# Optimization experiments

Hardware: AMD Instinct MI355X
Metric: run time of the kernel (lower is better)

## Reference

```python
import jax, jax.numpy as jnp
import numpy as np
import math

B, L, D, E, H = 8, 128, 512, 64, 8
SLOPE = 0.2
EPS = 1e-5


def setup_inputs() -> dict:
    key = jax.random.key(0)
    ks = jax.random.split(key, 10)
    s = 0.02
    x = jax.random.normal(ks[0], (B, L, D), jnp.float32)
    adj = jax.random.randint(ks[1], (B, L, L), 0, 2, jnp.int32)  # 0/1 adjacency
    e = jax.random.normal(ks[2], (B, L, L, E), jnp.float32)
    Wq = jax.random.normal(ks[3], (D, D), jnp.float32) * s
    Wkv = jax.random.normal(ks[4], (D, D), jnp.float32) * s
    We = jax.random.normal(ks[5], (E, D), jnp.float32) * s
    Wf = jax.random.normal(ks[6], (D, D), jnp.float32) * s
    bf = jnp.zeros((D,), jnp.float32)
    gamma = jnp.ones((D,), jnp.float32)
    beta = jnp.zeros((D,), jnp.float32)
    return {"x": x, "adj": adj, "e": e, "Wq": Wq, "Wkv": Wkv, "We": We,
            "Wf": Wf, "bf": bf, "gamma": gamma, "beta": beta}


def reference(x, adj, e, Wq, Wkv, We, Wf, bf, gamma, beta):
    C = D // H
    # projections
    q = (x @ Wq).reshape(B, L, H, C).transpose(0, 2, 1, 3)    # (B,H,L,C)
    kv = (x @ Wkv).reshape(B, L, H, C).transpose(0, 2, 1, 3)  # (B,H,L,C)
    ee = (e @ We).reshape(B, L, L, H, C).transpose(0, 3, 1, 2, 4)  # (B,H,Lq,Lk,C)
    # edge-modulated value/key: depends on both query and key position
    kve = kv[:, :, None, :, :] + ee                            # (B,H,Lq,Lk,C)
    # scores
    alpha = jnp.einsum('bhqc,bhqkc->bhqk', q, kve) / math.sqrt(C)
    alpha = jax.nn.leaky_relu(alpha, SLOPE)
    mask = (adj != 0)[:, None, :, :]                           # (B,1,Lq,Lk)
    alpha = jnp.where(mask, alpha, jnp.float32(-1e9))
    alpha = jax.nn.softmax(alpha, axis=-1)                     # over keys
    # weighted sum of edge-modulated values
    out = jnp.einsum('bhqk,bhqkc->bhqc', alpha, kve)           # (B,H,L,C)
    out = out.transpose(0, 2, 1, 3).reshape(B, L, D)
    # FFN: Linear -> LayerNorm -> ReLU
    out = out @ Wf + bf
    mu = out.mean(-1, keepdims=True)
    var = ((out - mu) ** 2).mean(-1, keepdims=True)
    out = (out - mu) / jnp.sqrt(var + EPS) * gamma + beta
    return jax.nn.relu(out)
```

## Files before the change

kernel.cpp:

```cpp
#include <hip/hip_runtime.h>
#include <hip/hip_bf16.h>
#include <math.h>

#define BB 8
#define LL 128
#define DD 512
#define EE 64
#define HH 8
#define CC 64
#define SLOPE 0.2f
#define EPS 1e-5f

typedef short bf16x8v __attribute__((ext_vector_type(8)));
typedef float f32x4v __attribute__((ext_vector_type(4)));

static __device__ __forceinline__ unsigned short f2bf(float f) {
    union { float f; unsigned u; } v; v.f = f;
    unsigned r = v.u + 0x7FFFu + ((v.u >> 16) & 1u);
    return (unsigned short)(r >> 16);
}

__global__ __launch_bounds__(256) void pack_all(
    const float* __restrict__ x, const float* __restrict__ Wq,
    const float* __restrict__ Wkv, const float* __restrict__ Wf,
    const float* __restrict__ We,
    unsigned short* __restrict__ xb, unsigned short* __restrict__ Wqkv_t,
    unsigned short* __restrict__ Wf_t, unsigned short* __restrict__ We_bf,
    unsigned short* __restrict__ WeT_bf)
{
    const int blk = blockIdx.x, tid = threadIdx.x;
    if (blk < 256) {
        const int j = blk * 512 + tid * 2;
        #pragma unroll
        for (int i = 0; i < 2; ++i) {
            const float4 v = ((const float4*)x)[j + i];
            ushort4 u; u.x = f2bf(v.x); u.y = f2bf(v.y); u.z = f2bf(v.z); u.w = f2bf(v.w);
            ((ushort4*)xb)[j + i] = u;
        }
    } else if (blk < 1024) {
        __shared__ float tile[32][33];
        const int matId = (blk - 256) >> 8;
        const int t = (blk - 256) & 255;
        const float* src = matId == 0 ? Wq : (matId == 1 ? Wkv : Wf);
        unsigned short* dst = matId == 0 ? Wqkv_t : (matId == 1 ? Wqkv_t + DD * DD : Wf_t);
        const int xx = tid & 31, yy = tid >> 5;
        const int r0 = (t >> 4) * 32, c0 = (t & 15) * 32;
        #pragma unroll
        for (int j = 0; j < 32; j += 8)
            tile[yy + j][xx] = src[(r0 + yy + j) * DD + c0 + xx];
        __syncthreads();
        #pragma unroll
        for (int j = 0; j < 32; j += 8)
            dst[(c0 + yy + j) * DD + r0 + xx] = f2bf(tile[xx][yy + j]);
    } else if (blk < 1040) {
        const int j = (blk - 1024) * 512 + tid * 2;
        #pragma unroll
        for (int i = 0; i < 2; ++i) {
            const float4 v = ((const float4*)We)[j + i];
            ushort4 u; u.x = f2bf(v.x); u.y = f2bf(v.y); u.z = f2bf(v.z); u.w = f2bf(v.w);
            ((ushort4*)We_bf)[j + i] = u;
        }
    } else {
        __shared__ float tile[32][33];
        const int t = blk - 1040;
        const int xx = tid & 31, yy = tid >> 5;
        const int r0 = (t >> 4) * 32, c0 = (t & 15) * 32;
        #pragma unroll
        for (int j = 0; j < 32; j += 8)
            tile[yy + j][xx] = We[(r0 + yy + j) * DD + c0 + xx];
        __syncthreads();
        #pragma unroll
        for (int j = 0; j < 32; j += 8)
            WeT_bf[(c0 + yy + j) * EE + r0 + xx] = f2bf(tile[xx][yy + j]);
    }
}

__global__ __launch_bounds__(256) void proj_gemm(
    const unsigned short* __restrict__ A, const unsigned short* __restrict__ Bm,
    unsigned short* __restrict__ Q_bf, unsigned short* __restrict__ KV_bf,
    unsigned short* __restrict__ KVT_bf)
{
    const int wave = threadIdx.x >> 6, lane = threadIdx.x & 63;
    const int quad = lane >> 4, l16 = lane & 15;
    const int m0 = blockIdx.y * 64 + wave * 16;
    const int n0 = blockIdx.x * 64;
    const bf16x8v* Ap = (const bf16x8v*)(A + (m0 + l16) * DD) + quad;
    const bf16x8v* Bp = (const bf16x8v*)(Bm + (n0 + l16) * DD) + quad;
    f32x4v acc0 = {0.f,0.f,0.f,0.f}, acc1 = acc0, acc2 = acc0, acc3 = acc0;
    #pragma unroll 4
    for (int k = 0; k < 16; ++k) {
        const bf16x8v a = Ap[k * 4];
        acc0 = __builtin_amdgcn_mfma_f32_16x16x32_bf16(a, Bp[k * 4       ], acc0, 0, 0, 0);
        acc1 = __builtin_amdgcn_mfma_f32_16x16x32_bf16(a, Bp[k * 4 + 1024], acc1, 0, 0, 0);
        acc2 = __builtin_amdgcn_mfma_f32_16x16x32_bf16(a, Bp[k * 4 + 2048], acc2, 0, 0, 0);
        acc3 = __builtin_amdgcn_mfma_f32_16x16x32_bf16(a, Bp[k * 4 + 3072], acc3, 0, 0, 0);
    }
    const f32x4v accs[4] = {acc0, acc1, acc2, acc3};
    const int gm0 = m0 + quad * 4;
    #pragma unroll
    for (int t = 0; t < 4; ++t) {
        const int gn = n0 + t * 16 + l16;
        const int mat = gn >> 9, d = gn & 511, h = d >> 6, c = d & 63;
        unsigned short* dst = mat ? KV_bf : Q_bf;
        ushort4 pk;
        pk.x = f2bf(accs[t][0]); pk.y = f2bf(accs[t][1]);
        pk.z = f2bf(accs[t][2]); pk.w = f2bf(accs[t][3]);
        dst[(gm0 + 0) * DD + d] = pk.x;
        dst[(gm0 + 1) * DD + d] = pk.y;
        dst[(gm0 + 2) * DD + d] = pk.z;
        dst[(gm0 + 3) * DD + d] = pk.w;
        if (mat) {
            const int b = gm0 >> 7, l0 = gm0 & 127;
            *(ushort4*)&KVT_bf[(((b * HH + h) * CC + c) << 7) + l0] = pk;
        }
    }
}

__global__ __launch_bounds__(256) void qk_t_gemm(
    const unsigned short* __restrict__ Q_bf, const unsigned short* __restrict__ KV_bf,
    const unsigned short* __restrict__ We_bf,
    float* __restrict__ S1, unsigned short* __restrict__ T_bf)
{
    const int wave = threadIdx.x >> 6, lane = threadIdx.x & 63;
    const int quad = lane >> 4, l16 = lane & 15;
    const int bid = blockIdx.x;
    f32x4v acc[4];
    #pragma unroll
    for (int t = 0; t < 4; ++t) acc[t] = (f32x4v){0.f,0.f,0.f,0.f};

    if (bid < 256) {
        const int batch = bid >> 2, sub = bid & 3;
        const int b = batch >> 3, h = batch & 7;
        const int q0 = (sub >> 1) * 64 + wave * 16;
        const int k0 = (sub & 1) * 64;
        const unsigned short* Ap = Q_bf + (b * LL + q0 + l16) * DD + h * CC + quad * 8;
        #pragma unroll
        for (int ks = 0; ks < 2; ++ks) {
            const bf16x8v a = *(const bf16x8v*)(Ap + ks * 32);
            #pragma unroll
            for (int t = 0; t < 4; ++t) {
                const bf16x8v bb = *(const bf16x8v*)(KV_bf + (b * LL + k0 + t * 16 + l16) * DD + h * CC + quad * 8 + ks * 32);
                acc[t] = __builtin_amdgcn_mfma_f32_16x16x32_bf16(a, bb, acc[t], 0, 0, 0);
            }
        }
        #pragma unroll
        for (int t = 0; t < 4; ++t)
            #pragma unroll
            for (int r = 0; r < 4; ++r)
                S1[((batch * LL + q0 + quad * 4 + r) << 7) + k0 + t * 16 + l16] = acc[t][r];
    } else {
        const int bid2 = bid - 256;
        const int h = bid2 >> 4;
        const int m0 = (bid2 & 15) * 64 + wave * 16;
        const unsigned short* Ap = Q_bf + (m0 + l16) * DD + h * CC + quad * 8;
        #pragma unroll
        for (int ks = 0; ks < 2; ++ks) {
            const bf16x8v a = *(const bf16x8v*)(Ap + ks * 32);
            #pragma unroll
            for (int t = 0; t < 4; ++t) {
                const bf16x8v bb = *(const bf16x8v*)(We_bf + (t * 16 + l16) * DD + h * CC + quad * 8 + ks * 32);
                acc[t] = __builtin_amdgcn_mfma_f32_16x16x32_bf16(a, bb, acc[t], 0, 0, 0);
            }
        }
        #pragma unroll
        for (int t = 0; t < 4; ++t)
            #pragma unroll
            for (int r = 0; r < 4; ++r)
                T_bf[(m0 + quad * 4 + r) * DD + h * CC + t * 16 + l16] = f2bf(acc[t][r]);
    }
}

#define ES 72
#define ETS 136
__global__ __launch_bounds__(256) void attn_fused(
    const float* __restrict__ e, const int* __restrict__ adj,
    const float* __restrict__ S1, const unsigned short* __restrict__ T_bf,
    unsigned short* __restrict__ P1, unsigned short* __restrict__ G_bf)
{
    __shared__ unsigned short lds_e[LL * ES];
    __shared__ unsigned short lds_eT[EE * ETS];
    __shared__ float s_lds[HH * 132];
    __shared__ unsigned short p_bf[HH * ETS];

    const int bq = blockIdx.x;
    const int b = bq >> 7, q = bq & 127;
    const int tid = threadIdx.x;
    const int wave = tid >> 6, lane = tid & 63, quad = lane >> 4, l16 = lane & 15;

    const float4* e4 = (const float4*)(e + (size_t)bq * (LL * EE));
    #pragma unroll
    for (int rep = 0; rep < 8; ++rep) {
        const int j = rep * 256 + tid;
        const float4 v = e4[j];
        const int k = j >> 4, x0 = (j & 15) * 4;
        ushort4 u; u.x = f2bf(v.x); u.y = f2bf(v.y); u.z = f2bf(v.z); u.w = f2bf(v.w);
        *(ushort4*)&lds_e[k * ES + x0] = u;
        lds_eT[(x0    ) * ETS + k] = u.x;
        lds_eT[(x0 + 1) * ETS + k] = u.y;
        lds_eT[(x0 + 2) * ETS + k] = u.z;
        lds_eT[(x0 + 3) * ETS + k] = u.w;
    }
    __syncthreads();

    const int hh = l16 < 8 ? l16 : 7;
    const unsigned short* Trow = T_bf + bq * DD + hh * CC + quad * 8;
    const bf16x8v tb0 = *(const bf16x8v*)(Trow);
    const bf16x8v tb1 = *(const bf16x8v*)(Trow + 32);
    f32x4v sacc[2];
    #pragma unroll
    for (int mt = 0; mt < 2; ++mt) {
        sacc[mt] = (f32x4v){0.f,0.f,0.f,0.f};
        const int kb = wave * 32 + mt * 16;
        const bf16x8v a0 = *(const bf16x8v*)&lds_e[(kb + l16) * ES + quad * 8];
        const bf16x8v a1 = *(const bf16x8v*)&lds_e[(kb + l16) * ES + 32 + quad * 8];
        sacc[mt] = __builtin_amdgcn_mfma_f32_16x16x32_bf16(a0, tb0, sacc[mt], 0, 0, 0);
        sacc[mt] = __builtin_amdgcn_mfma_f32_16x16x32_bf16(a1, tb1, sacc[mt], 0, 0, 0);
    }
    if (l16 < 8) {
        #pragma unroll
        for (int mt = 0; mt < 2; ++mt) {
            const int kk0 = wave * 32 + mt * 16 + quad * 4;
            const float4 s1v = *(const float4*)&S1[(((b * HH + l16) * LL + q) << 7) + kk0];
            const int4 av = *(const int4*)&adj[bq * LL + kk0];
            float sv[4] = {s1v.x, s1v.y, s1v.z, s1v.w};
            const int am[4] = {av.x, av.y, av.z, av.w};
            float4 o;
            float* op = (float*)&o;
            #pragma unroll
            for (int r = 0; r < 4; ++r) {
                float sc = (sv[r] + sacc[mt][r]) * 0.125f;
                sc = (sc >= 0.f) ? sc : SLOPE * sc;
                op[r] = (am[r] == 0) ? -1e9f : sc;
            }
            *(float4*)&s_lds[l16 * 132 + kk0] = o;
        }
    }
    __syncthreads();

    {
        const int h = tid >> 5, t5 = tid & 31;
        float m = -INFINITY;
        #pragma unroll
        for (int i = 0; i < 4; ++i) m = fmaxf(m, s_lds[h * 132 + t5 + i * 32]);
        #pragma unroll
        for (int off = 16; off > 0; off >>= 1) m = fmaxf(m, __shfl_down(m, off, 32));
        m = __shfl(m, 0, 32);
        const int k0 = t5 * 4;
        float ev[4];
        #pragma unroll
        for (int i = 0; i < 4; ++i) ev[i] = expf(s_lds[h * 132 + k0 + i] - m);
        float l = ev[0] + ev[1] + ev[2] + ev[3];
        #pragma unroll
        for (int off = 16; off > 0; off >>= 1) l += __shfl_down(l, off, 32);
        l = __shfl(l, 0, 32);
        const float inv = 1.f / l;
        ushort4 pk;
        pk.x = f2bf(ev[0] * inv); pk.y = f2bf(ev[1] * inv);
        pk.z = f2bf(ev[2] * inv); pk.w = f2bf(ev[3] * inv);
        *(ushort4*)&p_bf[h * ETS + k0] = pk;
        *(ushort4*)&P1[(((b * HH + h) * LL + q) << 7) + k0] = pk;
    }
    __syncthreads();

    {
        const int hr = l16 < 8 ? l16 : 0;
        f32x4v g = {0.f,0.f,0.f,0.f};
        #pragma unroll
        for (int ks = 0; ks < 4; ++ks) {
            const bf16x8v a  = *(const bf16x8v*)&p_bf[hr * ETS + ks * 32 + quad * 8];
            const bf16x8v bb = *(const bf16x8v*)&lds_eT[(wave * 16 + l16) * ETS + ks * 32 + quad * 8];
            g = __builtin_amdgcn_mfma_f32_16x16x32_bf16(a, bb, g, 0, 0, 0);
        }
        if (quad < 2) {
            #pragma unroll
            for (int r = 0; r < 4; ++r)
                G_bf[bq * DD + (quad * 4 + r) * CC + wave * 16 + l16] = f2bf(g[r]);
        }
    }
}

__global__ __launch_bounds__(256) void pv_gemm(
    const unsigned short* __restrict__ P1, const unsigned short* __restrict__ KVT_bf,
    float* __restrict__ O1)
{
    const int wave = threadIdx.x >> 6, lane = threadIdx.x & 63;
    const int quad = lane >> 4, l16 = lane & 15;
    const int batch = blockIdx.x >> 1;
    const int q0 = (blockIdx.x & 1) * 64 + wave * 16;
    const int b = batch >> 3, h = batch & 7;
    f32x4v acc[4];
    #pragma unroll
    for (int t = 0; t < 4; ++t) acc[t] = (f32x4v){0.f,0.f,0.f,0.f};
    const unsigned short* Ap = P1 + ((batch * LL + q0 + l16) << 7) + quad * 8;
    #pragma unroll
    for (int ks = 0; ks < 4; ++ks) {
        const bf16x8v a = *(const bf16x8v*)(Ap + ks * 32);
        #pragma unroll
        for (int t = 0; t < 4; ++t) {
            const bf16x8v bb = *(const bf16x8v*)(KVT_bf + (((batch * CC + t * 16 + l16)) << 7) + quad * 8 + ks * 32);
            acc[t] = __builtin_amdgcn_mfma_f32_16x16x32_bf16(a, bb, acc[t], 0, 0, 0);
        }
    }
    #pragma unroll
    for (int t = 0; t < 4; ++t)
        #pragma unroll
        for (int r = 0; r < 4; ++r)
            O1[(b * LL + q0 + quad * 4 + r) * DD + h * CC + t * 16 + l16] = acc[t][r];
}

__global__ __launch_bounds__(256) void o2_gemm(
    const unsigned short* __restrict__ G_bf, const unsigned short* __restrict__ WeT_bf,
    const float* __restrict__ O1, unsigned short* __restrict__ attn_bf)
{
    const int wave = threadIdx.x >> 6, lane = threadIdx.x & 63;
    const int quad = lane >> 4, l16 = lane & 15;
    const int h = blockIdx.x >> 4;
    const int m0 = (blockIdx.x & 15) * 64 + wave * 16;
    f32x4v acc[4];
    #pragma unroll
    for (int t = 0; t < 4; ++t) acc[t] = (f32x4v){0.f,0.f,0.f,0.f};
    const unsigned short* Ap = G_bf + (m0 + l16) * DD + h * CC + quad * 8;
    #pragma unroll
    for (int ks = 0; ks < 2; ++ks) {
        const bf16x8v a = *(const bf16x8v*)(Ap + ks * 32);
        #pragma unroll
        for (int t = 0; t < 4; ++t) {
            const bf16x8v bb = *(const bf16x8v*)(WeT_bf + (h * CC + t * 16 + l16) * EE + quad * 8 + ks * 32);
            acc[t] = __builtin_amdgcn_mfma_f32_16x16x32_bf16(a, bb, acc[t], 0, 0, 0);
        }
    }
    #pragma unroll
    for (int t = 0; t < 4; ++t) {
        const int d = h * CC + t * 16 + l16;
        #pragma unroll
        for (int r = 0; r < 4; ++r) {
            const int row = m0 + quad * 4 + r;
            attn_bf[row * DD + d] = f2bf(acc[t][r] + O1[row * DD + d]);
        }
    }
}

__global__ __launch_bounds__(256) void ffn_gemm(
    const unsigned short* __restrict__ A, const unsigned short* __restrict__ Bm,
    const float* __restrict__ bfv, float* __restrict__ vals)
{
    const int wave = threadIdx.x >> 6, lane = threadIdx.x & 63;
    const int quad = lane >> 4, l16 = lane & 15;
    const int m0 = blockIdx.y * 64 + wave * 16;
    const int n0 = blockIdx.x * 64;
    const bf16x8v* Ap = (const bf16x8v*)(A + (m0 + l16) * DD) + quad;
    const bf16x8v* Bp = (const bf16x8v*)(Bm + (n0 + l16) * DD) + quad;
    f32x4v acc0 = {0.f,0.f,0.f,0.f}, acc1 = acc0, acc2 = acc0, acc3 = acc0;
    #pragma unroll 4
    for (int k = 0; k < 16; ++k) {
        const bf16x8v a = Ap[k * 4];
        acc0 = __builtin_amdgcn_mfma_f32_16x16x32_bf16(a, Bp[k * 4       ], acc0, 0, 0, 0);
        acc1 = __builtin_amdgcn_mfma_f32_16x16x32_bf16(a, Bp[k * 4 + 1024], acc1, 0, 0, 0);
        acc2 = __builtin_amdgcn_mfma_f32_16x16x32_bf16(a, Bp[k * 4 + 2048], acc2, 0, 0, 0);
        acc3 = __builtin_amdgcn_mfma_f32_16x16x32_bf16(a, Bp[k * 4 + 3072], acc3, 0, 0, 0);
    }
    const f32x4v accs[4] = {acc0, acc1, acc2, acc3};
    #pragma unroll
    for (int t = 0; t < 4; ++t) {
        const int gn = n0 + t * 16 + l16;
        const float bias = bfv[gn];
        #pragma unroll
        for (int r = 0; r < 4; ++r)
            vals[(m0 + quad * 4 + r) * DD + gn] = accs[t][r] + bias;
    }
}

__global__ __launch_bounds__(256) void ln_kernel(
    const float* __restrict__ vals, const float* __restrict__ gamma,
    const float* __restrict__ beta, float* __restrict__ out)
{
    __shared__ float red[8];
    __shared__ float stats[2];
    const int row = blockIdx.x;
    const int tid = threadIdx.x;
    const float v0 = vals[row * DD + tid];
    const float v1 = vals[row * DD + tid + 256];
    float ls = v0 + v1;
    float lss = v0 * v0 + v1 * v1;
    #pragma unroll
    for (int off = 32; off > 0; off >>= 1) {
        ls += __shfl_down(ls, off);
        lss += __shfl_down(lss, off);
    }
    const int wid = tid >> 6;
    if ((tid & 63) == 0) { red[wid * 2] = ls; red[wid * 2 + 1] = lss; }
    __syncthreads();
    if (tid == 0) {
        float ts = 0.f, tss = 0.f;
        for (int w = 0; w < 4; ++w) { ts += red[w * 2]; tss += red[w * 2 + 1]; }
        const float mu = ts / (float)DD;
        const float var = tss / (float)DD - mu * mu;
        stats[0] = mu;
        stats[1] = rsqrtf(var + EPS);
    }
    __syncthreads();
    const float mu = stats[0], rsig = stats[1];
    const float o0 = (v0 - mu) * rsig * gamma[tid] + beta[tid];
    const float o1 = (v1 - mu) * rsig * gamma[tid + 256] + beta[tid + 256];
    out[row * DD + tid] = fmaxf(o0, 0.f);
    out[row * DD + tid + 256] = fmaxf(o1, 0.f);
}

extern "C" void kernel_launch(void* const* d_in, const int* in_sizes, int n_in,
                              void* d_out, int out_size, void* d_ws, size_t ws_size,
                              hipStream_t stream)
{
    const float* x    = (const float*)d_in[0];
    const int*   adj  = (const int*)  d_in[1];
    const float* e    = (const float*)d_in[2];
    const float* Wq   = (const float*)d_in[3];
    const float* Wkv  = (const float*)d_in[4];
    const float* We   = (const float*)d_in[5];
    const float* Wf   = (const float*)d_in[6];
    const float* bf   = (const float*)d_in[7];
    const float* gam  = (const float*)d_in[8];
    const float* bet  = (const float*)d_in[9];
    float* out = (float*)d_out;

    const int MROW = BB * LL;
    char* w = (char*)d_ws;
    unsigned short* Q_bf   = (unsigned short*)(w);
    unsigned short* KV_bf  = (unsigned short*)(w + (1u  << 20));
    unsigned short* KVT_bf = (unsigned short*)(w + (2u  << 20));
    float*          S1     = (float*)         (w + (3u  << 20));
    unsigned short* T_bf   = (unsigned short*)(w + (7u  << 20));
    unsigned short* P1     = (unsigned short*)(w + (8u  << 20));
    unsigned short* G_bf   = (unsigned short*)(w + (10u << 20));
    float*          O1     = (float*)         (w + (11u << 20));
    float*          vals   = (float*)         (w + (13u << 20));
    unsigned short* xb     = (unsigned short*)(w + (15u << 20));
    unsigned short* Wqkv_t = (unsigned short*)(w + (16u << 20));
    unsigned short* Wf_t   = (unsigned short*)(w + (17u << 20));
    unsigned short* We_bf  = (unsigned short*)(w + (17u << 20) + (512u << 10));
    unsigned short* WeT_bf = (unsigned short*)(w + (17u << 20) + (576u << 10));

    pack_all<<<1072, 256, 0, stream>>>(x, Wq, Wkv, Wf, We, xb, Wqkv_t, Wf_t, We_bf, WeT_bf);
    proj_gemm<<<dim3(16, 16), 256, 0, stream>>>(xb, Wqkv_t, Q_bf, KV_bf, KVT_bf);
    qk_t_gemm<<<384, 256, 0, stream>>>(Q_bf, KV_bf, We_bf, S1, T_bf);
    attn_fused<<<MROW, 256, 0, stream>>>(e, adj, S1, T_bf, P1, G_bf);
    pv_gemm<<<128, 256, 0, stream>>>(P1, KVT_bf, O1);
    o2_gemm<<<128, 256, 0, stream>>>(G_bf, WeT_bf, O1, (unsigned short*)Q_bf );
    ffn_gemm<<<dim3(8, 16), 256, 0, stream>>>((unsigned short*)Q_bf, Wf_t, bf, vals);
    ln_kernel<<<MROW, 256, 0, stream>>>(vals, gam, bet, out);
}
```

Measured before the change: 140.1 us.

## Fold Wq·We into projection GEMM and fuse PV/O2 and FFN/LayerNorm kernels

Precomputes Wq·We^T per head in the pack kernel and appends it as extra columns of the projection GEMM, so T comes straight from x instead of from a separate GEMM on Q. Merges the PV and edge-output GEMMs into one kernel that accumulates both in registers. Fuses the FFN GEMM with the LayerNorm and ReLU using in-block row reductions. Drops the transposed e copy in LDS and gathers it with strided LDS reads instead. The intent is fewer launches and fewer intermediate round trips through global memory, at the cost of scalar FP32 weight precompute work, a different bf16 rounding order, and an FFN kernel launched on only 64 blocks.

```diff
diff --git a/kernel.cpp b/kernel.cpp
--- a/kernel.cpp
+++ b/kernel.cpp
@@ -24,9 +24,8 @@
     const float* __restrict__ x, const float* __restrict__ Wq,
     const float* __restrict__ Wkv, const float* __restrict__ Wf,
     const float* __restrict__ We,
-    unsigned short* __restrict__ xb, unsigned short* __restrict__ Wqkv_t,
-    unsigned short* __restrict__ Wf_t, unsigned short* __restrict__ We_bf,
-    unsigned short* __restrict__ WeT_bf)
+    unsigned short* __restrict__ xb, unsigned short* __restrict__ Ball,
+    unsigned short* __restrict__ Wf_t, unsigned short* __restrict__ WeT_bf)
 {
     const int blk = blockIdx.x, tid = threadIdx.x;
     if (blk < 256) {
@@ -42,7 +41,7 @@
         const int matId = (blk - 256) >> 8;
         const int t = (blk - 256) & 255;
         const float* src = matId == 0 ? Wq : (matId == 1 ? Wkv : Wf);
-        unsigned short* dst = matId == 0 ? Wqkv_t : (matId == 1 ? Wqkv_t + DD * DD : Wf_t);
+        unsigned short* dst = matId == 0 ? Ball : (matId == 1 ? Ball + DD * DD : Wf_t);
         const int xx = tid & 31, yy = tid >> 5;
         const int r0 = (t >> 4) * 32, c0 = (t & 15) * 32;
         #pragma unroll
@@ -52,17 +51,9 @@
         #pragma unroll
         for (int j = 0; j < 32; j += 8)
             dst[(c0 + yy + j) * DD + r0 + xx] = f2bf(tile[xx][yy + j]);
-    } else if (blk < 1040) {
-        const int j = (blk - 1024) * 512 + tid * 2;
-        #pragma unroll
-        for (int i = 0; i < 2; ++i) {
-            const float4 v = ((const float4*)We)[j + i];
-            ushort4 u; u.x = f2bf(v.x); u.y = f2bf(v.y); u.z = f2bf(v.z); u.w = f2bf(v.w);
-            ((ushort4*)We_bf)[j + i] = u;
-        }
-    } else {
+    } else if (blk < 1056) {
         __shared__ float tile[32][33];
-        const int t = blk - 1040;
+        const int t = blk - 1024;
         const int xx = tid & 31, yy = tid >> 5;
         const int r0 = (t >> 4) * 32, c0 = (t & 15) * 32;
         #pragma unroll
@@ -72,13 +63,40 @@
         #pragma unroll
         for (int j = 0; j < 32; j += 8)
             WeT_bf[(c0 + yy + j) * EE + r0 + xx] = f2bf(tile[xx][yy + j]);
+    } else {
+        __shared__ float weRows[4][64];
+        const int hx0 = (blk - 1056) * 4;
+        const int ridx = tid >> 6;
+        const int r = hx0 + ridx;
+        const int h = r >> 6, xr = r & 63;
+        {
+            const int c = tid & 63;
+            weRows[ridx][c] = We[xr * DD + h * CC + c];
+        }
+        __syncthreads();
+        const int d0 = (tid & 63) * 8;
+        float acc[8] = {0.f,0.f,0.f,0.f,0.f,0.f,0.f,0.f};
+        #pragma unroll 4
+        for (int c4 = 0; c4 < 16; ++c4) {
+            const float4 w4 = *(const float4*)&weRows[ridx][c4 * 4];
+            #pragma unroll
+            for (int i = 0; i < 8; ++i) {
+                const float4 q4 = *(const float4*)&Wq[(d0 + i) * DD + h * CC + c4 * 4];
+                acc[i] += q4.x * w4.x + q4.y * w4.y + q4.z * w4.z + q4.w * w4.w;
+            }
+        }
+        ushort4 lo, hi;
+        lo.x = f2bf(acc[0]); lo.y = f2bf(acc[1]); lo.z = f2bf(acc[2]); lo.w = f2bf(acc[3]);
+        hi.x = f2bf(acc[4]); hi.y = f2bf(acc[5]); hi.z = f2bf(acc[6]); hi.w = f2bf(acc[7]);
+        *(ushort4*)&Ball[(1024 + r) * DD + d0]     = lo;
+        *(ushort4*)&Ball[(1024 + r) * DD + d0 + 4] = hi;
     }
 }
 
 __global__ __launch_bounds__(256) void proj_gemm(
     const unsigned short* __restrict__ A, const unsigned short* __restrict__ Bm,
     unsigned short* __restrict__ Q_bf, unsigned short* __restrict__ KV_bf,
-    unsigned short* __restrict__ KVT_bf)
+    unsigned short* __restrict__ KVT_bf, unsigned short* __restrict__ T_bf)
 {
     const int wave = threadIdx.x >> 6, lane = threadIdx.x & 63;
     const int quad = lane >> 4, l16 = lane & 15;
@@ -100,74 +118,60 @@
     #pragma unroll
     for (int t = 0; t < 4; ++t) {
         const int gn = n0 + t * 16 + l16;
-        const int mat = gn >> 9, d = gn & 511, h = d >> 6, c = d & 63;
-        unsigned short* dst = mat ? KV_bf : Q_bf;
         ushort4 pk;
         pk.x = f2bf(accs[t][0]); pk.y = f2bf(accs[t][1]);
         pk.z = f2bf(accs[t][2]); pk.w = f2bf(accs[t][3]);
-        dst[(gm0 + 0) * DD + d] = pk.x;
-        dst[(gm0 + 1) * DD + d] = pk.y;
-        dst[(gm0 + 2) * DD + d] = pk.z;
-        dst[(gm0 + 3) * DD + d] = pk.w;
-        if (mat) {
+        if (gn < 512) {
+            Q_bf[(gm0 + 0) * DD + gn] = pk.x;
+            Q_bf[(gm0 + 1) * DD + gn] = pk.y;
+            Q_bf[(gm0 + 2) * DD + gn] = pk.z;
+            Q_bf[(gm0 + 3) * DD + gn] = pk.w;
+        } else if (gn < 1024) {
+            const int d = gn - 512, h = d >> 6, c = d & 63;
+            KV_bf[(gm0 + 0) * DD + d] = pk.x;
+            KV_bf[(gm0 + 1) * DD + d] = pk.y;
+            KV_bf[(gm0 + 2) * DD + d] = pk.z;
+            KV_bf[(gm0 + 3) * DD + d] = pk.w;
             const int b = gm0 >> 7, l0 = gm0 & 127;
             *(ushort4*)&KVT_bf[(((b * HH + h) * CC + c) << 7) + l0] = pk;
-        }
-    }
-}
-
-__global__ __launch_bounds__(256) void qk_t_gemm(
+        } else {
+            const int d = gn - 1024;
+            T_bf[(gm0 + 0) * DD + d] = pk.x;
+            T_bf[(gm0 + 1) * DD + d] = pk.y;
+            T_bf[(gm0 + 2) * DD + d] = pk.z;
+            T_bf[(gm0 + 3) * DD + d] = pk.w;
+        }
+    }
+}
+
+__global__ __launch_bounds__(256) void qk_gemm(
     const unsigned short* __restrict__ Q_bf, const unsigned short* __restrict__ KV_bf,
-    const unsigned short* __restrict__ We_bf,
-    float* __restrict__ S1, unsigned short* __restrict__ T_bf)
+    float* __restrict__ S1)
 {
     const int wave = threadIdx.x >> 6, lane = threadIdx.x & 63;
     const int quad = lane >> 4, l16 = lane & 15;
-    const int bid = blockIdx.x;
+    const int batch = blockIdx.x >> 2, sub = blockIdx.x & 3;
+    const int b = batch >> 3, h = batch & 7;
+    const int q0 = (sub >> 1) * 64 + wave * 16;
+    const int k0 = (sub & 1) * 64;
     f32x4v acc[4];
     #pragma unroll
     for (int t = 0; t < 4; ++t) acc[t] = (f32x4v){0.f,0.f,0.f,0.f};
-
-    if (bid < 256) {
-        const int batch = bid >> 2, sub = bid & 3;
-        const int b = batch >> 3, h = batch & 7;
-        const int q0 = (sub >> 1) * 64 + wave * 16;
-        const int k0 = (sub & 1) * 64;
-        const unsigned short* Ap = Q_bf + (b * LL + q0 + l16) * DD + h * CC + quad * 8;
-        #pragma unroll
-        for (int ks = 0; ks < 2; ++ks) {
-            const bf16x8v a = *(const bf16x8v*)(Ap + ks * 32);
-            #pragma unroll
-            for (int t = 0; t < 4; ++t) {
-                const bf16x8v bb = *(const bf16x8v*)(KV_bf + (b * LL + k0 + t * 16 + l16) * DD + h * CC + quad * 8 + ks * 32);
-                acc[t] = __builtin_amdgcn_mfma_f32_16x16x32_bf16(a, bb, acc[t], 0, 0, 0);
-            }
-        }
-        #pragma unroll
-        for (int t = 0; t < 4; ++t)
-            #pragma unroll
-            for (int r = 0; r < 4; ++r)
-                S1[((batch * LL + q0 + quad * 4 + r) << 7) + k0 + t * 16 + l16] = acc[t][r];
-    } else {
-        const int bid2 = bid - 256;
-        const int h = bid2 >> 4;
-        const int m0 = (bid2 & 15) * 64 + wave * 16;
-        const unsigned short* Ap = Q_bf + (m0 + l16) * DD + h * CC + quad * 8;
-        #pragma unroll
-        for (int ks = 0; ks < 2; ++ks) {
-            const bf16x8v a = *(const bf16x8v*)(Ap + ks * 32);
-            #pragma unroll
-            for (int t = 0; t < 4; ++t) {
-                const bf16x8v bb = *(const bf16x8v*)(We_bf + (t * 16 + l16) * DD + h * CC + quad * 8 + ks * 32);
-                acc[t] = __builtin_amdgcn_mfma_f32_16x16x32_bf16(a, bb, acc[t], 0, 0, 0);
-            }
-        }
-        #pragma unroll
-        for (int t = 0; t < 4; ++t)
-            #pragma unroll
-            for (int r = 0; r < 4; ++r)
-                T_bf[(m0 + quad * 4 + r) * DD + h * CC + t * 16 + l16] = f2bf(acc[t][r]);
-    }
+    const unsigned short* Ap = Q_bf + (b * LL + q0 + l16) * DD + h * CC + quad * 8;
+    #pragma unroll
+    for (int ks = 0; ks < 2; ++ks) {
+        const bf16x8v a = *(const bf16x8v*)(Ap + ks * 32);
+        #pragma unroll
+        for (int t = 0; t < 4; ++t) {
+            const bf16x8v bb = *(const bf16x8v*)(KV_bf + (b * LL + k0 + t * 16 + l16) * DD + h * CC + quad * 8 + ks * 32);
+            acc[t] = __builtin_amdgcn_mfma_f32_16x16x32_bf16(a, bb, acc[t], 0, 0, 0);
+        }
+    }
+    #pragma unroll
+    for (int t = 0; t < 4; ++t)
+        #pragma unroll
+        for (int r = 0; r < 4; ++r)
+            S1[((batch * LL + q0 + quad * 4 + r) << 7) + k0 + t * 16 + l16] = acc[t][r];
 }
 
 #define ES 72
@@ -178,7 +182,6 @@
     unsigned short* __restrict__ P1, unsigned short* __restrict__ G_bf)
 {
     __shared__ unsigned short lds_e[LL * ES];
-    __shared__ unsigned short lds_eT[EE * ETS];
     __shared__ float s_lds[HH * 132];
     __shared__ unsigned short p_bf[HH * ETS];
 
@@ -195,10 +198,6 @@
         const int k = j >> 4, x0 = (j & 15) * 4;
         ushort4 u; u.x = f2bf(v.x); u.y = f2bf(v.y); u.z = f2bf(v.z); u.w = f2bf(v.w);
         *(ushort4*)&lds_e[k * ES + x0] = u;
-        lds_eT[(x0    ) * ETS + k] = u.x;
-        lds_eT[(x0 + 1) * ETS + k] = u.y;
-        lds_eT[(x0 + 2) * ETS + k] = u.z;
-        lds_eT[(x0 + 3) * ETS + k] = u.w;
     }
     __syncthreads();
 
@@ -222,10 +221,9 @@
             const int kk0 = wave * 32 + mt * 16 + quad * 4;
             const float4 s1v = *(const float4*)&S1[(((b * HH + l16) * LL + q) << 7) + kk0];
             const int4 av = *(const int4*)&adj[bq * LL + kk0];
-            float sv[4] = {s1v.x, s1v.y, s1v.z, s1v.w};
+            const float sv[4] = {s1v.x, s1v.y, s1v.z, s1v.w};
             const int am[4] = {av.x, av.y, av.z, av.w};
-            float4 o;
-            float* op = (float*)&o;
+            float4 o; float* op = (float*)&o;
             #pragma unroll
             for (int r = 0; r < 4; ++r) {
                 float sc = (sv[r] + sacc[mt][r]) * 0.125f;
@@ -267,8 +265,11 @@
         f32x4v g = {0.f,0.f,0.f,0.f};
         #pragma unroll
         for (int ks = 0; ks < 4; ++ks) {
-            const bf16x8v a  = *(const bf16x8v*)&p_bf[hr * ETS + ks * 32 + quad * 8];
-            const bf16x8v bb = *(const bf16x8v*)&lds_eT[(wave * 16 + l16) * ETS + ks * 32 + quad * 8];
+            const bf16x8v a = *(const bf16x8v*)&p_bf[hr * ETS + ks * 32 + quad * 8];
+            bf16x8v bb;
+            #pragma unroll
+            for (int j = 0; j < 8; ++j)
+                bb[j] = (short)lds_e[(ks * 32 + quad * 8 + j) * ES + wave * 16 + l16];
             g = __builtin_amdgcn_mfma_f32_16x16x32_bf16(a, bb, g, 0, 0, 0);
         }
         if (quad < 2) {
@@ -279,9 +280,10 @@
     }
 }
 
-__global__ __launch_bounds__(256) void pv_gemm(
+__global__ __launch_bounds__(256) void out_gemm(
     const unsigned short* __restrict__ P1, const unsigned short* __restrict__ KVT_bf,
-    float* __restrict__ O1)
+    const unsigned short* __restrict__ G_bf, const unsigned short* __restrict__ WeT_bf,
+    unsigned short* __restrict__ attn_bf)
 {
     const int wave = threadIdx.x >> 6, lane = threadIdx.x & 63;
     const int quad = lane >> 4, l16 = lane & 15;
@@ -291,119 +293,111 @@
     f32x4v acc[4];
     #pragma unroll
     for (int t = 0; t < 4; ++t) acc[t] = (f32x4v){0.f,0.f,0.f,0.f};
+
     const unsigned short* Ap = P1 + ((batch * LL + q0 + l16) << 7) + quad * 8;
     #pragma unroll
     for (int ks = 0; ks < 4; ++ks) {
         const bf16x8v a = *(const bf16x8v*)(Ap + ks * 32);
         #pragma unroll
         for (int t = 0; t < 4; ++t) {
-            const bf16x8v bb = *(const bf16x8v*)(KVT_bf + (((batch * CC + t * 16 + l16)) << 7) + quad * 8 + ks * 32);
+            const bf16x8v bb = *(const bf16x8v*)(KVT_bf + ((batch * CC + t * 16 + l16) << 7) + ks * 32 + quad * 8);
             acc[t] = __builtin_amdgcn_mfma_f32_16x16x32_bf16(a, bb, acc[t], 0, 0, 0);
         }
     }
+    const unsigned short* Ap2 = G_bf + (b * LL + q0 + l16) * DD + h * CC + quad * 8;
+    #pragma unroll
+    for (int ks = 0; ks < 2; ++ks) {
+        const bf16x8v a = *(const bf16x8v*)(Ap2 + ks * 32);
+        #pragma unroll
+        for (int t = 0; t < 4; ++t) {
+            const bf16x8v bb = *(const bf16x8v*)(WeT_bf + (h * CC + t * 16 + l16) * EE + ks * 32 + quad * 8);
+            acc[t] = __builtin_amdgcn_mfma_f32_16x16x32_bf16(a, bb, acc[t], 0, 0, 0);
+        }
+    }
     #pragma unroll
     for (int t = 0; t < 4; ++t)
         #pragma unroll
         for (int r = 0; r < 4; ++r)
-            O1[(b * LL + q0 + quad * 4 + r) * DD + h * CC + t * 16 + l16] = acc[t][r];
-}
-
-__global__ __launch_bounds__(256) void o2_gemm(
-    const unsigned short* __restrict__ G_bf, const unsigned short* __restrict__ WeT_bf,
-    const float* __restrict__ O1, unsigned short* __restrict__ attn_bf)
-{
+            attn_bf[(b * LL + q0 + quad * 4 + r) * DD + h * CC + t * 16 + l16] = f2bf(acc[t][r]);
+}
+
+__global__ __launch_bounds__(256) void ffn_ln(
+    const unsigned short* __restrict__ A, const unsigned short* __restrict__ Bm,
+    const float* __restrict__ bfv, const float* __restrict__ gamma,
+    const float* __restrict__ beta, float* __restrict__ out)
+{
+    __shared__ float red_s[4][16];
+    __shared__ float red_ss[4][16];
+    __shared__ float st_mu[16];
+    __shared__ float st_rs[16];
+
     const int wave = threadIdx.x >> 6, lane = threadIdx.x & 63;
     const int quad = lane >> 4, l16 = lane & 15;
-    const int h = blockIdx.x >> 4;
-    const int m0 = (blockIdx.x & 15) * 64 + wave * 16;
-    f32x4v acc[4];
-    #pragma unroll
-    for (int t = 0; t < 4; ++t) acc[t] = (f32x4v){0.f,0.f,0.f,0.f};
-    const unsigned short* Ap = G_bf + (m0 + l16) * DD + h * CC + quad * 8;
-    #pragma unroll
-    for (int ks = 0; ks < 2; ++ks) {
-        const bf16x8v a = *(const bf16x8v*)(Ap + ks * 32);
-        #pragma unroll
-        for (int t = 0; t < 4; ++t) {
-            const bf16x8v bb = *(const bf16x8v*)(WeT_bf + (h * CC + t * 16 + l16) * EE + quad * 8 + ks * 32);
+    const int m0 = blockIdx.x * 16;
+    f32x4v acc[8];
+    #pragma unroll
+    for (int t = 0; t < 8; ++t) acc[t] = (f32x4v){0.f,0.f,0.f,0.f};
+
+    const unsigned short* Ap = A + (m0 + l16) * DD + quad * 8;
+    #pragma unroll 2
+    for (int k = 0; k < 16; ++k) {
+        const bf16x8v a = *(const bf16x8v*)(Ap + k * 32);
+        #pragma unroll
+        for (int t = 0; t < 8; ++t) {
+            const bf16x8v bb = *(const bf16x8v*)(Bm + (wave * 128 + t * 16 + l16) * DD + k * 32 + quad * 8);
             acc[t] = __builtin_amdgcn_mfma_f32_16x16x32_bf16(a, bb, acc[t], 0, 0, 0);
         }
     }
-    #pragma unroll
-    for (int t = 0; t < 4; ++t) {
-        const int d = h * CC + t * 16 + l16;
+    float ps[4] = {0.f,0.f,0.f,0.f}, pss[4] = {0.f,0.f,0.f,0.f};
+    #pragma unroll
+    for (int t = 0; t < 8; ++t) {
+        const float bias = bfv[wave * 128 + t * 16 + l16];
         #pragma unroll
         for (int r = 0; r < 4; ++r) {
-            const int row = m0 + quad * 4 + r;
-            attn_bf[row * DD + d] = f2bf(acc[t][r] + O1[row * DD + d]);
-        }
-    }
-}
-
-__global__ __launch_bounds__(256) void ffn_gemm(
-    const unsigned short* __restrict__ A, const unsigned short* __restrict__ Bm,
-    const float* __restrict__ bfv, float* __restrict__ vals)
-{
-    const int wave = threadIdx.x >> 6, lane = threadIdx.x & 63;
-    const int quad = lane >> 4, l16 = lane & 15;
-    const int m0 = blockIdx.y * 64 + wave * 16;
-    const int n0 = blockIdx.x * 64;
-    const bf16x8v* Ap = (const bf16x8v*)(A + (m0 + l16) * DD) + quad;
-    const bf16x8v* Bp = (const bf16x8v*)(Bm + (n0 + l16) * DD) + quad;
-    f32x4v acc0 = {0.f,0.f,0.f,0.f}, acc1 = acc0, acc2 = acc0, acc3 = acc0;
-    #pragma unroll 4
-    for (int k = 0; k < 16; ++k) {
-        const bf16x8v a = Ap[k * 4];
-        acc0 = __builtin_amdgcn_mfma_f32_16x16x32_bf16(a, Bp[k * 4       ], acc0, 0, 0, 0);
-        acc1 = __builtin_amdgcn_mfma_f32_16x16x32_bf16(a, Bp[k * 4 + 1024], acc1, 0, 0, 0);
-        acc2 = __builtin_amdgcn_mfma_f32_16x16x32_bf16(a, Bp[k * 4 + 2048], acc2, 0, 0, 0);
-        acc3 = __builtin_amdgcn_mfma_f32_16x16x32_bf16(a, Bp[k * 4 + 3072], acc3, 0, 0, 0);
-    }
-    const f32x4v accs[4] = {acc0, acc1, acc2, acc3};
-    #pragma unroll
-    for (int t = 0; t < 4; ++t) {
-        const int gn = n0 + t * 16 + l16;
-        const float bias = bfv[gn];
-        #pragma unroll
-        for (int r = 0; r < 4; ++r)
-            vals[(m0 + quad * 4 + r) * DD + gn] = accs[t][r] + bias;
-    }
-}
-
-__global__ __launch_bounds__(256) void ln_kernel(
-    const float* __restrict__ vals, const float* __restrict__ gamma,
-    const float* __restrict__ beta, float* __restrict__ out)
-{
-    __shared__ float red[8];
-    __shared__ float stats[2];
-    const int row = blockIdx.x;
-    const int tid = threadIdx.x;
-    const float v0 = vals[row * DD + tid];
-    const float v1 = vals[row * DD + tid + 256];
-    float ls = v0 + v1;
-    float lss = v0 * v0 + v1 * v1;
-    #pragma unroll
-    for (int off = 32; off > 0; off >>= 1) {
-        ls += __shfl_down(ls, off);
-        lss += __shfl_down(lss, off);
-    }
-    const int wid = tid >> 6;
-    if ((tid & 63) == 0) { red[wid * 2] = ls; red[wid * 2 + 1] = lss; }
+            const float v = acc[t][r] + bias;
+            acc[t][r] = v;
+            ps[r] += v;
+            pss[r] += v * v;
+        }
+    }
+    #pragma unroll
+    for (int off = 1; off < 16; off <<= 1) {
+        #pragma unroll
+        for (int r = 0; r < 4; ++r) {
+            ps[r]  += __shfl_xor(ps[r],  off, 16);
+            pss[r] += __shfl_xor(pss[r], off, 16);
+        }
+    }
+    if (l16 == 0) {
+        #pragma unroll
+        for (int r = 0; r < 4; ++r) {
+            red_s[wave][quad * 4 + r]  = ps[r];
+            red_ss[wave][quad * 4 + r] = pss[r];
+        }
+    }
     __syncthreads();
-    if (tid == 0) {
+    if (threadIdx.x < 16) {
+        const int row = threadIdx.x;
         float ts = 0.f, tss = 0.f;
-        for (int w = 0; w < 4; ++w) { ts += red[w * 2]; tss += red[w * 2 + 1]; }
+        #pragma unroll
+        for (int w = 0; w < 4; ++w) { ts += red_s[w][row]; tss += red_ss[w][row]; }
         const float mu = ts / (float)DD;
         const float var = tss / (float)DD - mu * mu;
-        stats[0] = mu;
-        stats[1] = rsqrtf(var + EPS);
+        st_mu[row] = mu;
+        st_rs[row] = rsqrtf(var + EPS);
     }
     __syncthreads();
-    const float mu = stats[0], rsig = stats[1];
-    const float o0 = (v0 - mu) * rsig * gamma[tid] + beta[tid];
-    const float o1 = (v1 - mu) * rsig * gamma[tid + 256] + beta[tid + 256];
-    out[row * DD + tid] = fmaxf(o0, 0.f);
-    out[row * DD + tid + 256] = fmaxf(o1, 0.f);
+    #pragma unroll
+    for (int r = 0; r < 4; ++r) {
+        const int row = quad * 4 + r;
+        const float mu = st_mu[row], rs = st_rs[row];
+        #pragma unroll
+        for (int t = 0; t < 8; ++t) {
+            const int gn = wave * 128 + t * 16 + l16;
+            const float o = (acc[t][r] - mu) * rs * gamma[gn] + beta[gn];
+            out[(m0 + row) * DD + gn] = fmaxf(o, 0.f);
+        }
+    }
 }
 
 extern "C" void kernel_launch(void* const* d_in, const int* in_sizes, int n_in,
@@ -424,27 +418,23 @@
 
     const int MROW = BB * LL;
     char* w = (char*)d_ws;
-    unsigned short* Q_bf   = (unsigned short*)(w);
-    unsigned short* KV_bf  = (unsigned short*)(w + (1u  << 20));
-    unsigned short* KVT_bf = (unsigned short*)(w + (2u  << 20));
-    float*          S1     = (float*)         (w + (3u  << 20));
-    unsigned short* T_bf   = (unsigned short*)(w + (7u  << 20));
-    unsigned short* P1     = (unsigned short*)(w + (8u  << 20));
-    unsigned short* G_bf   = (unsigned short*)(w + (10u << 20));
-    float*          O1     = (float*)         (w + (11u << 20));
-    float*          vals   = (float*)         (w + (13u << 20));
-    unsigned short* xb     = (unsigned short*)(w + (15u << 20));
-    unsigned short* Wqkv_t = (unsigned short*)(w + (16u << 20));
-    unsigned short* Wf_t   = (unsigned short*)(w + (17u << 20));
-    unsigned short* We_bf  = (unsigned short*)(w + (17u << 20) + (512u << 10));
-    unsigned short* WeT_bf = (unsigned short*)(w + (17u << 20) + (576u << 10));
-
-    pack_all<<<1072, 256, 0, stream>>>(x, Wq, Wkv, Wf, We, xb, Wqkv_t, Wf_t, We_bf, WeT_bf);
-    proj_gemm<<<dim3(16, 16), 256, 0, stream>>>(xb, Wqkv_t, Q_bf, KV_bf, KVT_bf);
-    qk_t_gemm<<<384, 256, 0, stream>>>(Q_bf, KV_bf, We_bf, S1, T_bf);
+    unsigned short* Ball    = (unsigned short*)(w);
+    unsigned short* xb      = (unsigned short*)(w + (2u  << 20));
+    unsigned short* Q_bf    = (unsigned short*)(w + (3u  << 20));
+    unsigned short* KV_bf   = (unsigned short*)(w + (4u  << 20));
+    unsigned short* KVT_bf  = (unsigned short*)(w + (5u  << 20));
+    unsigned short* T_bf    = (unsigned short*)(w + (6u  << 20));
+    float*          S1      = (float*)         (w + (7u  << 20));
+    unsigned short* P1      = (unsigned short*)(w + (11u << 20));
+    unsigned short* G_bf    = (unsigned short*)(w + (13u << 20));
+    unsigned short* attn_bf = (unsigned short*)(w + (14u << 20));
+    unsigned short* WeT_bf  = (unsigned short*)(w + (15u << 20));
+    unsigned short* Wf_t    = (unsigned short*)(w + (16u << 20));
+
+    pack_all<<<1184, 256, 0, stream>>>(x, Wq, Wkv, Wf, We, xb, Ball, Wf_t, WeT_bf);
+    proj_gemm<<<dim3(24, 16), 256, 0, stream>>>(xb, Ball, Q_bf, KV_bf, KVT_bf, T_bf);
+    qk_gemm<<<256, 256, 0, stream>>>(Q_bf, KV_bf, S1);
     attn_fused<<<MROW, 256, 0, stream>>>(e, adj, S1, T_bf, P1, G_bf);
-    pv_gemm<<<128, 256, 0, stream>>>(P1, KVT_bf, O1);
-    o2_gemm<<<128, 256, 0, stream>>>(G_bf, WeT_bf, O1, (unsigned short*)Q_bf );
-    ffn_gemm<<<dim3(8, 16), 256, 0, stream>>>((unsigned short*)Q_bf, Wf_t, bf, vals);
-    ln_kernel<<<MROW, 256, 0, stream>>>(vals, gam, bet, out);
-}
+    out_gemm<<<128, 256, 0, stream>>>(P1, KVT_bf, G_bf, WeT_bf, attn_bf);
+    ffn_ln<<<64, 256, 0, stream>>>(attn_bf, Wf_t, bf, gam, bet, out);
+}
```

Result: slower. 186.4 us (+33.1%).
